# Kernel tuning notes

Measured on AMD Instinct MI355X. Metric: run time of the kernel, lower is better.

The kernel has to match this reference:

```python
import jax, jax.numpy as jnp
import numpy as np
import math

L, D, H = 4, 256, 8
HD = D // H
B, SQ, SK = 2, 1024, 1024
FF = 3 * D
EPS = 1e-5


def setup_inputs() -> dict:
    key = jax.random.key(0)
    ks = jax.random.split(key, 16)
    s = 0.02
    w = lambda k, shape: jax.random.normal(k, shape, jnp.float32) * s
    return {
        "pose": jax.random.normal(ks[0], (B, SQ, D), jnp.float32),
        "vel": jax.random.normal(ks[1], (B, SK, D), jnp.float32),
        "img": jax.random.normal(ks[2], (B, SK, D), jnp.float32),
        "Wq": w(ks[3], (L, D, D)), "bq": jnp.zeros((L, D), jnp.float32),
        "Wk": w(ks[4], (L, D, D)), "bk": jnp.zeros((L, D), jnp.float32),
        "Wv": w(ks[5], (L, D, D)), "bv": jnp.zeros((L, D), jnp.float32),
        "Wo": w(ks[6], (L, D, D)), "bo": jnp.zeros((L, D), jnp.float32),
        "an_g": jnp.ones((L, D), jnp.float32), "an_b": jnp.zeros((L, D), jnp.float32),
        "W1": w(ks[7], (L, D, FF)), "b1": jnp.zeros((L, FF), jnp.float32),
        "W2": w(ks[8], (L, FF, D)), "b2": jnp.zeros((L, D), jnp.float32),
        "fn_g": jnp.ones((L, D), jnp.float32), "fn_b": jnp.zeros((L, D), jnp.float32),
        "n_g": jnp.ones((L, D), jnp.float32), "n_b": jnp.zeros((L, D), jnp.float32),
    }


def entmax15(x):
    # exact alpha=1.5 entmax along the last axis (Peters & Martins 2019)
    x = x * 0.5
    x = x - jnp.max(x, axis=-1, keepdims=True)
    z = -jnp.sort(-x, axis=-1)  # descending
    k = jnp.arange(1, z.shape[-1] + 1, dtype=x.dtype)
    mean = jnp.cumsum(z, axis=-1) / k
    mean_sq = jnp.cumsum(z * z, axis=-1) / k
    ss = k * (mean_sq - mean * mean)
    delta = jnp.clip((1.0 - ss) / k, 0.0)
    tau = mean - jnp.sqrt(delta)
    support = jnp.sum(tau <= z, axis=-1, keepdims=True)  # support size >= 1
    tau_star = jnp.take_along_axis(tau, support - 1, axis=-1)
    p = jnp.clip(x - tau_star, 0.0)
    return p * p


def layer_norm(x, g, b):
    m = jnp.mean(x, axis=-1, keepdims=True)
    v = jnp.mean((x - m) ** 2, axis=-1, keepdims=True)
    return (x - m) * jax.lax.rsqrt(v + EPS) * g + b


def mish(x):
    return x * jnp.tanh(jax.nn.softplus(x))


def reference(pose, vel, img, Wq, bq, Wk, bk, Wv, bv, Wo, bo, an_g, an_b,
              W1, b1, W2, b2, fn_g, fn_b, n_g, n_b):
    def mha(q_in, kv, i):
        bs, sq, _ = q_in.shape
        sk = kv.shape[1]
        q = (q_in @ Wq[i] + bq[i]).reshape(bs, sq, H, HD)
        k = (kv @ Wk[i] + bk[i]).reshape(bs, sk, H, HD)
        v = (kv @ Wv[i] + bv[i]).reshape(bs, sk, H, HD)
        scores = jnp.einsum('bqhd,bkhd->bhqk', q, k) / math.sqrt(HD)
        attn = entmax15(scores)
        out = jnp.einsum('bhqk,bkhd->bqhd', attn, v).reshape(bs, sq, D)
        return out @ Wo[i] + bo[i]

    def cross_layer(x1, x2, i):
        y = layer_norm(mha(x1, x2, i), an_g[i], an_b[i])
        x1 = x1 + y
        y = layer_norm(x1, fn_g[i], fn_b[i])
        h = mish(y @ W1[i] + b1[i]) @ W2[i] + b2[i]
        return x1 + h

    def stack(x, kv):
        for i in range(L):  # small fixed layer loop (shared weights across both paths)
            mem = x
            x = cross_layer(x, kv, i)
            x = layer_norm(x, n_g[i], n_b[i])
            x = x + mem
        return x

    img_out = stack(pose, img)
    pose_out = stack(pose, vel)
    return (pose_out, img_out)
```

## Files before the change

kernel.cpp:

```cpp
#include <hip/hip_runtime.h>
#include <math.h>

#define NL   4
#define DIM  256
#define NH   8
#define HDIM 32
#define SQL  1024
#define SKL  1024
#define FFD  768
#define CB   4
#define ROWS (CB * SQL)

typedef __attribute__((ext_vector_type(8))) short bf16x8;
typedef __attribute__((ext_vector_type(4))) short bf16x4;
typedef __attribute__((ext_vector_type(4))) float f32x4;
typedef __attribute__((ext_vector_type(2))) float f32x2;


__device__ __forceinline__ short f2bf(float f) {
    union { float f; unsigned u; } v; v.f = f;
    unsigned u = v.u + 0x7fffu + ((v.u >> 16) & 1u);
    return (short)(u >> 16);
}

__device__ __forceinline__ float fast_mish(float x) {
    float u = __expf(fminf(x, 20.0f));
    float a = __builtin_fmaf(u, u, 2.0f * u);
    return x * a * __builtin_amdgcn_rcpf(a + 2.0f);
}

__device__ __forceinline__ f32x2 lo2(f32x4 v) { return __builtin_shufflevector(v, v, 0, 1); }
__device__ __forceinline__ f32x2 hi2(f32x4 v) { return __builtin_shufflevector(v, v, 2, 3); }


__global__ __launch_bounds__(256) void init_kernel(
        const float* __restrict__ pose, const float* __restrict__ vel,
        const float* __restrict__ img, float* __restrict__ X,
        short* __restrict__ Xb, short* __restrict__ KVb) {
    int idx = blockIdx.x * 256 + threadIdx.x;
    if (idx >= CB * SQL * DIM) return;
    int c = idx / (SQL * DIM);
    int rem = idx - c * (SQL * DIM);
    int b = c & 1;
    float pv = pose[b * SQL * DIM + rem];
    X[idx]  = pv;
    Xb[idx] = f2bf(pv);
    const float* kv = (c < 2) ? vel : img;
    KVb[idx] = f2bf(kv[b * SQL * DIM + rem]);
}


__global__ __launch_bounds__(256) void transpose_all(
        const float* __restrict__ Wq, const float* __restrict__ Wk,
        const float* __restrict__ Wv, const float* __restrict__ Wo,
        const float* __restrict__ W1, const float* __restrict__ W2,
        short* __restrict__ Wqt, short* __restrict__ Wkt,
        short* __restrict__ Wvt, short* __restrict__ Wot,
        short* __restrict__ W1t, short* __restrict__ W2t) {
    __shared__ float tile[64][65];
    int z = blockIdx.x;
    const float* src; short* dst; int K, N, tx, ty;
    if (z < 256) {
        int m = z >> 6, lyr = (z >> 4) & 3, r = z & 15;
        src = ((m == 0) ? Wq : (m == 1) ? Wk : (m == 2) ? Wv : Wo) + (size_t)lyr * DIM * DIM;
        dst = ((m == 0) ? Wqt : (m == 1) ? Wkt : (m == 2) ? Wvt : Wot) + (size_t)lyr * DIM * DIM;
        K = DIM; N = DIM; tx = r & 3; ty = r >> 2;
    } else if (z < 448) {
        int idx = z - 256, lyr = idx / 48, r = idx % 48;
        src = W1 + (size_t)lyr * DIM * FFD; dst = W1t + (size_t)lyr * DIM * FFD;
        K = DIM; N = FFD; tx = r % 12; ty = r / 12;
    } else {
        int idx = z - 448, lyr = idx / 48, r = idx % 48;
        src = W2 + (size_t)lyr * FFD * DIM; dst = W2t + (size_t)lyr * FFD * DIM;
        K = FFD; N = DIM; tx = r % 4; ty = r / 4;
    }
    int t = threadIdx.x;
    int n0 = tx * 64, k0 = ty * 64;
#pragma unroll
    for (int i = 0; i < 16; i++) {
        int idx = t + i * 256;
        int r = idx >> 6, c = idx & 63;
        tile[r][c] = src[(size_t)(k0 + r) * N + n0 + c];
    }
    __syncthreads();
#pragma unroll
    for (int i = 0; i < 16; i++) {
        int idx = t + i * 256;
        int r = idx >> 6, c = idx & 63;
        dst[(size_t)(n0 + r) * K + k0 + c] = f2bf(tile[c][r]);
    }
}


__global__ __launch_bounds__(256) void qkv_gemm(
        const short* __restrict__ Xb, const short* __restrict__ KVb,
        const short* __restrict__ Wqt, const short* __restrict__ Wkt,
        const short* __restrict__ Wvt,
        const float* __restrict__ bq, const float* __restrict__ bk,
        const float* __restrict__ bv,
        short* __restrict__ Qb, short* __restrict__ Kb, short* __restrict__ Vt,
        float qscale) {
    int z = blockIdx.z;
    const short* A    = (z == 0) ? Xb : KVb;
    const short* Wt   = (z == 0) ? Wqt : (z == 1) ? Wkt : Wvt;
    const float* bias = (z == 0) ? bq : (z == 1) ? bk : bv;
    float scale = (z == 0) ? qscale : 1.0f;

    int t = threadIdx.x, l = t & 63, w = t >> 6;
    int lq = l & 15, lg = l >> 4;
    int bm = blockIdx.y * 64, bn = blockIdx.x * 64;

    const short* ap = A + (size_t)(bm + w * 16 + lq) * DIM + lg * 8;
    const short* wp = Wt + (size_t)(bn + lq) * DIM + lg * 8;

    f32x4 acc[4];
#pragma unroll
    for (int nt = 0; nt < 4; nt++) acc[nt] = (f32x4){0.f, 0.f, 0.f, 0.f};
#pragma unroll
    for (int k0 = 0; k0 < DIM; k0 += 32) {
        bf16x8 af = *(const bf16x8*)(ap + k0);
#pragma unroll
        for (int nt = 0; nt < 4; nt++) {
            bf16x8 bfr = *(const bf16x8*)(wp + (size_t)nt * 16 * DIM + k0);
            acc[nt] = __builtin_amdgcn_mfma_f32_16x16x32_bf16(af, bfr, acc[nt], 0, 0, 0);
        }
    }

    int ms = bm + w * 16 + lg * 4;
#pragma unroll
    for (int nt = 0; nt < 4; nt++) {
        int col = bn + nt * 16 + lq;
        float bv_ = bias[col];
        float v[4];
#pragma unroll
        for (int j = 0; j < 4; j++) v[j] = acc[nt][j] + bv_;
        if (z < 2) {
            short* out = (z == 0) ? Qb : Kb;
#pragma unroll
            for (int j = 0; j < 4; j++) out[(size_t)(ms + j) * DIM + col] = f2bf(v[j] * scale);
        } else {
            int cc = ms >> 10, kl = ms & 1023;
            bf16x4 pk;
#pragma unroll
            for (int j = 0; j < 4; j++) pk[j] = f2bf(v[j]);
            *(bf16x4*)(Vt + ((size_t)(cc * DIM + col)) * SKL + kl) = pk;
        }
    }
}


__global__ __launch_bounds__(512) void gemm_ln2(
        const short* __restrict__ A, const short* __restrict__ Wt,
        const float* __restrict__ bias, const float* __restrict__ Xres,
        const float* __restrict__ ag, const float* __restrict__ ab,
        const float* __restrict__ fg, const float* __restrict__ fb,
        float* __restrict__ x1out, short* __restrict__ yout) {
    __shared__ float gbuf[16][264];
    int t = threadIdx.x, l = t & 63, w = t >> 6;
    int lq = l & 15, lg = l >> 4;
    int bm = blockIdx.x * 16;

    const short* ap = A + (size_t)(bm + lq) * DIM + lg * 8;
    const short* wp = Wt + (size_t)(w * 32 + lq) * DIM + lg * 8;

    f32x4 acc[2];
    acc[0] = (f32x4){0.f, 0.f, 0.f, 0.f};
    acc[1] = (f32x4){0.f, 0.f, 0.f, 0.f};
#pragma unroll
    for (int k0 = 0; k0 < DIM; k0 += 32) {
        bf16x8 af = *(const bf16x8*)(ap + k0);
#pragma unroll
        for (int nt = 0; nt < 2; nt++) {
            bf16x8 bfr = *(const bf16x8*)(wp + (size_t)nt * 16 * DIM + k0);
            acc[nt] = __builtin_amdgcn_mfma_f32_16x16x32_bf16(af, bfr, acc[nt], 0, 0, 0);
        }
    }
#pragma unroll
    for (int nt = 0; nt < 2; nt++) {
        int col = w * 32 + nt * 16 + lq;
        float bv_ = bias[col];
#pragma unroll
        for (int j = 0; j < 4; j++) gbuf[lg * 4 + j][col] = acc[nt][j] + bv_;
    }
    __syncthreads();

    int g = t >> 5, u = t & 31;
    int row = bm + g;
    float s = 0.f, s2 = 0.f;
#pragma unroll
    for (int i = 0; i < 8; i++) {
        float v = gbuf[g][u + 32 * i];
        s += v; s2 += v * v;
    }
#pragma unroll
    for (int off = 1; off < 32; off <<= 1) { s += __shfl_xor(s, off); s2 += __shfl_xor(s2, off); }
    float m = s * (1.f / DIM);
    float rstd = rsqrtf(s2 * (1.f / DIM) - m * m + 1e-5f);

    float x1v[8];
    float sb = 0.f, sb2 = 0.f;
#pragma unroll
    for (int i = 0; i < 8; i++) {
        int col = u + 32 * i;
        float x1 = Xres[(size_t)row * DIM + col] + (gbuf[g][col] - m) * rstd * ag[col] + ab[col];
        x1v[i] = x1; sb += x1; sb2 += x1 * x1;
    }
#pragma unroll
    for (int off = 1; off < 32; off <<= 1) { sb += __shfl_xor(sb, off); sb2 += __shfl_xor(sb2, off); }
    float m2 = sb * (1.f / DIM);
    float rstd2 = rsqrtf(sb2 * (1.f / DIM) - m2 * m2 + 1e-5f);
#pragma unroll
    for (int i = 0; i < 8; i++) {
        int col = u + 32 * i;
        x1out[(size_t)row * DIM + col] = x1v[i];
        yout[(size_t)row * DIM + col]  = f2bf((x1v[i] - m2) * rstd2 * fg[col] + fb[col]);
    }
}


__global__ __launch_bounds__(512) void gemm_ffn(
        const short* __restrict__ Yb, const short* __restrict__ W1t,
        const float* __restrict__ b1, const short* __restrict__ W2t,
        const float* __restrict__ b2, const float* __restrict__ x1res,
        const float* __restrict__ Xres, const float* __restrict__ g_,
        const float* __restrict__ b_,
        float* __restrict__ outf, short* __restrict__ outb) {
    __shared__ __align__(16) char lds[16 * 776 * 2];
    short (*g1)[776]   = (short(*)[776])lds;
    float (*gbuf)[264] = (float(*)[264])lds;

    int t = threadIdx.x, l = t & 63, w = t >> 6;
    int lq = l & 15, lg = l >> 4;
    int bm = blockIdx.x * 16;

    {
        const short* ap = Yb + (size_t)(bm + lq) * DIM + lg * 8;
        const short* wp = W1t + (size_t)(w * 96 + lq) * DIM + lg * 8;
        f32x4 acc[6];
#pragma unroll
        for (int nt = 0; nt < 6; nt++) acc[nt] = (f32x4){0.f, 0.f, 0.f, 0.f};
#pragma unroll
        for (int k0 = 0; k0 < DIM; k0 += 32) {
            bf16x8 af = *(const bf16x8*)(ap + k0);
#pragma unroll
            for (int nt = 0; nt < 6; nt++) {
                bf16x8 bfr = *(const bf16x8*)(wp + (size_t)nt * 16 * DIM + k0);
                acc[nt] = __builtin_amdgcn_mfma_f32_16x16x32_bf16(af, bfr, acc[nt], 0, 0, 0);
            }
        }
#pragma unroll
        for (int nt = 0; nt < 6; nt++) {
            int col = w * 96 + nt * 16 + lq;
            float bv_ = b1[col];
#pragma unroll
            for (int j = 0; j < 4; j++)
                g1[lg * 4 + j][col] = f2bf(fast_mish(acc[nt][j] + bv_));
        }
    }
    __syncthreads();

    f32x4 acc2[2];
    acc2[0] = (f32x4){0.f, 0.f, 0.f, 0.f};
    acc2[1] = (f32x4){0.f, 0.f, 0.f, 0.f};
    {
        const short* wp2 = W2t + (size_t)(w * 32 + lq) * FFD + lg * 8;
#pragma unroll 6
        for (int ks = 0; ks < 24; ks++) {
            bf16x8 af = *(const bf16x8*)(&g1[lq][ks * 32 + lg * 8]);
#pragma unroll
            for (int nt = 0; nt < 2; nt++) {
                bf16x8 bfr = *(const bf16x8*)(wp2 + (size_t)nt * 16 * FFD + ks * 32);
                acc2[nt] = __builtin_amdgcn_mfma_f32_16x16x32_bf16(af, bfr, acc2[nt], 0, 0, 0);
            }
        }
    }
    __syncthreads();

#pragma unroll
    for (int nt = 0; nt < 2; nt++) {
        int col = w * 32 + nt * 16 + lq;
        float bv_ = b2[col];
#pragma unroll
        for (int j = 0; j < 4; j++) {
            int row = bm + lg * 4 + j;
            gbuf[lg * 4 + j][col] = acc2[nt][j] + bv_ + x1res[(size_t)row * DIM + col];
        }
    }
    __syncthreads();

    int g = t >> 5, u = t & 31;
    int row = bm + g;
    float s = 0.f, s2 = 0.f;
#pragma unroll
    for (int i = 0; i < 8; i++) {
        float v = gbuf[g][u + 32 * i];
        s += v; s2 += v * v;
    }
#pragma unroll
    for (int off = 1; off < 32; off <<= 1) { s += __shfl_xor(s, off); s2 += __shfl_xor(s2, off); }
    float m = s * (1.f / DIM);
    float rstd = rsqrtf(s2 * (1.f / DIM) - m * m + 1e-5f);
#pragma unroll
    for (int i = 0; i < 8; i++) {
        int col = u + 32 * i;
        float o = Xres[(size_t)row * DIM + col] + (gbuf[g][col] - m) * rstd * g_[col] + b_[col];
        outf[(size_t)row * DIM + col] = o;
        if (outb) outb[(size_t)row * DIM + col] = f2bf(o);
    }
}


__global__ __launch_bounds__(256) void attn_mfma(
        const short* __restrict__ Q, const short* __restrict__ K,
        const short* __restrict__ Vt, short* __restrict__ O) {
    int h = blockIdx.y, c = blockIdx.z;
    int qbase = blockIdx.x * 16;
    int t = threadIdx.x, l = t & 63, w = t >> 6;
    int lq = l & 15, lg = l >> 4;

    __shared__ __align__(16) short p_lds[4][1024];
    __shared__ float obuf[4][512];
    __shared__ float redf[2][3][4][16];

    bf16x8 qfrag = *(const bf16x8*)(Q + ((size_t)(c * SQL + qbase + lq)) * DIM + h * HDIM + lg * 8);

    const int kw = w * 256;
    f32x4 acc[16];
#pragma unroll
    for (int kt = 0; kt < 16; kt++) {
        bf16x8 kf = *(const bf16x8*)(K + ((size_t)(c * SKL + kw + kt * 16 + lq)) * DIM + h * HDIM + lg * 8);
        f32x4 z = {0.f, 0.f, 0.f, 0.f};
        acc[kt] = __builtin_amdgcn_mfma_f32_16x16x32_bf16(kf, qfrag, z, 0, 0, 0);
    }

    const f32x2 z2  = {0.f, 0.f};
    const f32x2 big = {1e30f, 1e30f};
    const f32x2 one = {1.f, 1.f};

    f32x2 mm = lo2(acc[0]);
#pragma unroll
    for (int kt = 0; kt < 16; kt++) {
        mm = __builtin_elementwise_max(mm, lo2(acc[kt]));
        mm = __builtin_elementwise_max(mm, hi2(acc[kt]));
    }
    float m = fmaxf(mm.x, mm.y);
    m = fmaxf(m, __shfl_xor(m, 16));
    m = fmaxf(m, __shfl_xor(m, 32));
    if (l < 16) redf[1][0][w][l] = m;
    __syncthreads();
    m = fmaxf(fmaxf(redf[1][0][0][lq], redf[1][0][1][lq]),
              fmaxf(redf[1][0][2][lq], redf[1][0][3][lq]));

    float tau = m - 1.0f;
    int r = 0;
    for (;;) {
        f32x2 vt = {tau, tau};
        f32x2 S1 = z2, S2 = z2, NN = z2;
#pragma unroll
        for (int kt = 0; kt < 16; kt++) {
            f32x2 y0 = __builtin_elementwise_max(lo2(acc[kt]) - vt, z2);
            f32x2 y1 = __builtin_elementwise_max(hi2(acc[kt]) - vt, z2);
            S1 += y0; S1 += y1;
            S2 += y0 * y0; S2 += y1 * y1;
            NN += __builtin_elementwise_min(y0 * big, one);
            NN += __builtin_elementwise_min(y1 * big, one);
        }
        float sy = S1.x + S1.y, sy2 = S2.x + S2.y, nn = NN.x + NN.y;
        sy  += __shfl_xor(sy, 16);  sy  += __shfl_xor(sy, 32);
        sy2 += __shfl_xor(sy2, 16); sy2 += __shfl_xor(sy2, 32);
        nn  += __shfl_xor(nn, 16);  nn  += __shfl_xor(nn, 32);
        int b = r & 1;
        if (l < 16) { redf[b][0][w][l] = nn; redf[b][1][w][l] = sy; redf[b][2][w][l] = sy2; }
        __syncthreads();
        nn  = redf[b][0][0][lq] + redf[b][0][1][lq] + redf[b][0][2][lq] + redf[b][0][3][lq];
        sy  = redf[b][1][0][lq] + redf[b][1][1][lq] + redf[b][1][2][lq] + redf[b][1][3][lq];
        sy2 = redf[b][2][0][lq] + redf[b][2][1][lq] + redf[b][2][2][lq] + redf[b][2][3][lq];
        float disc = fmaxf(sy * sy - nn * (sy2 - 1.0f), 0.f);
        float delta = (sy - sqrtf(disc)) / nn;
        tau = fminf(tau + delta, m - 0.03125f);
        r++;
        if (r >= 6 || __all(delta < 1e-6f)) break;
    }

    f32x4 o0 = {0.f, 0.f, 0.f, 0.f}, o1 = {0.f, 0.f, 0.f, 0.f};
    const short* vbase0 = Vt + ((size_t)(c * DIM + h * HDIM + lq)) * SKL;
    const short* vbase1 = vbase0 + (size_t)16 * SKL;
    {
        f32x2 vt = {tau, tau};
        int swz = (lq & 7) << 4;
#pragma unroll
        for (int c2 = 0; c2 < 4; c2++) {
#pragma unroll
            for (int k4 = 0; k4 < 4; k4++) {
                int kt = c2 * 4 + k4;
                f32x2 y0 = __builtin_elementwise_max(lo2(acc[kt]) - vt, z2);
                f32x2 y1 = __builtin_elementwise_max(hi2(acc[kt]) - vt, z2);
                f32x2 p0 = y0 * y0, p1 = y1 * y1;
                unsigned u01, u23;
                asm("v_cvt_pk_bf16_f32 %0, %1, %2" : "=v"(u01) : "v"(p0.x), "v"(p0.y));
                asm("v_cvt_pk_bf16_f32 %0, %1, %2" : "=v"(u23) : "v"(p1.x), "v"(p1.y));
                int klocal = k4 * 16 + lg * 4;
                int byte = lq * 128 + ((klocal * 2) ^ swz);
                *(uint2*)((char*)p_lds[w] + byte) = make_uint2(u01, u23);
            }
#pragma unroll
            for (int k2 = 0; k2 < 2; k2++) {
                int klocal0 = k2 * 32 + lg * 8;
                int byte = lq * 128 + ((klocal0 * 2) ^ swz);
                bf16x8 pa = *(const bf16x8*)((const char*)p_lds[w] + byte);
                int k0 = kw + c2 * 64 + klocal0;
                bf16x8 vb0 = *(const bf16x8*)(vbase0 + k0);
                bf16x8 vb1 = *(const bf16x8*)(vbase1 + k0);
                o0 = __builtin_amdgcn_mfma_f32_16x16x32_bf16(pa, vb0, o0, 0, 0, 0);
                o1 = __builtin_amdgcn_mfma_f32_16x16x32_bf16(pa, vb1, o1, 0, 0, 0);
            }
        }
    }

#pragma unroll
    for (int j = 0; j < 4; j++) {
        obuf[w][(lg * 4 + j) * 32 + lq]      = o0[j];
        obuf[w][(lg * 4 + j) * 32 + 16 + lq] = o1[j];
    }
    __syncthreads();
#pragma unroll
    for (int rep = 0; rep < 2; rep++) {
        int e = t + rep * 256;
        int q = e >> 5, d = e & 31;
        float s = obuf[0][e] + obuf[1][e] + obuf[2][e] + obuf[3][e];
        O[((size_t)(c * SQL + qbase + q)) * DIM + h * HDIM + d] = f2bf(s);
    }
}


extern "C" void kernel_launch(void* const* d_in, const int* in_sizes, int n_in,
                              void* d_out, int out_size, void* d_ws, size_t ws_size,
                              hipStream_t stream) {
    const float* pose = (const float*)d_in[0];
    const float* vel  = (const float*)d_in[1];
    const float* img  = (const float*)d_in[2];
    const float* Wq   = (const float*)d_in[3];
    const float* bq   = (const float*)d_in[4];
    const float* Wk   = (const float*)d_in[5];
    const float* bk   = (const float*)d_in[6];
    const float* Wv   = (const float*)d_in[7];
    const float* bv   = (const float*)d_in[8];
    const float* Wo   = (const float*)d_in[9];
    const float* bo   = (const float*)d_in[10];
    const float* an_g = (const float*)d_in[11];
    const float* an_b = (const float*)d_in[12];
    const float* W1   = (const float*)d_in[13];
    const float* b1   = (const float*)d_in[14];
    const float* W2   = (const float*)d_in[15];
    const float* b2   = (const float*)d_in[16];
    const float* fn_g = (const float*)d_in[17];
    const float* fn_b = (const float*)d_in[18];
    const float* n_g  = (const float*)d_in[19];
    const float* n_b  = (const float*)d_in[20];

    const size_t SZ = (size_t)ROWS * DIM;
    float* X    = (float*)d_ws;
    float* X1b  = X + SZ;
    short* Xb   = (short*)(X1b + SZ);
    short* KVb  = Xb + SZ;
    short* T1b  = KVb + SZ;
    short* Qb   = T1b + SZ;
    short* Kb   = Qb + SZ;
    short* Vt   = Kb + SZ;
    short* Yb   = Vt + SZ;
    short* Wqt  = Yb + SZ;
    short* Wkt  = Wqt + (size_t)NL * DIM * DIM;
    short* Wvt  = Wkt + (size_t)NL * DIM * DIM;
    short* Wot  = Wvt + (size_t)NL * DIM * DIM;
    short* W1t  = Wot + (size_t)NL * DIM * DIM;
    short* W2t  = W1t + (size_t)NL * DIM * FFD;

    {
        int total = CB * SQL * DIM;
        init_kernel<<<(total + 255) / 256, 256, 0, stream>>>(pose, vel, img, X, Xb, KVb);
    }
    transpose_all<<<640, 256, 0, stream>>>(Wq, Wk, Wv, Wo, W1, W2,
                                           Wqt, Wkt, Wvt, Wot, W1t, W2t);

    const float qscale = 0.08838834764831845f;

    for (int i = 0; i < NL; i++) {
        const short* Wqt_i = Wqt + (size_t)i * DIM * DIM;
        const short* Wkt_i = Wkt + (size_t)i * DIM * DIM;
        const short* Wvt_i = Wvt + (size_t)i * DIM * DIM;
        const short* Wot_i = Wot + (size_t)i * DIM * DIM;
        const short* W1t_i = W1t + (size_t)i * DIM * FFD;
        const short* W2t_i = W2t + (size_t)i * DIM * FFD;

        qkv_gemm<<<dim3(DIM / 64, ROWS / 64, 3), 256, 0, stream>>>(
            Xb, KVb, Wqt_i, Wkt_i, Wvt_i,
            bq + i * DIM, bk + i * DIM, bv + i * DIM, Qb, Kb, Vt, qscale);

        attn_mfma<<<dim3(SQL / 16, NH, CB), 256, 0, stream>>>(Qb, Kb, Vt, T1b);

        gemm_ln2<<<ROWS / 16, 512, 0, stream>>>(
            T1b, Wot_i, bo + i * DIM, X,
            an_g + i * DIM, an_b + i * DIM, fn_g + i * DIM, fn_b + i * DIM,
            X1b, Yb);

        float* outp  = (i == NL - 1) ? (float*)d_out : X;
        short* outbp = (i == NL - 1) ? nullptr : Xb;
        gemm_ffn<<<ROWS / 16, 512, 0, stream>>>(
            Yb, W1t_i, b1 + i * FFD, W2t_i, b2 + i * DIM, X1b, X,
            n_g + i * DIM, n_b + i * DIM, outp, outbp);
    }

    (void)in_sizes; (void)n_in; (void)out_size; (void)ws_size;
}
```

Measured before the change: 415.2 us.

## Fuse out-projection LayerNorm and FFN into one tail kernel

Merges the Wo GEMM plus double LayerNorm kernel with the FFN kernel, keeping x1 and the normalized activations in LDS instead of round-tripping them through global memory. This removes one launch per layer and the X1b/Yb workspace traffic. The fused kernel uses more LDS per block, which may reduce occupancy. The attention kernel also gets a launch_bounds occupancy hint of 4.

New measurement: 388.5 us. 1.07x faster.

```diff
diff --git a/kernel.cpp b/kernel.cpp
--- a/kernel.cpp
+++ b/kernel.cpp
@@ -149,99 +149,92 @@
 }
 
 
-__global__ __launch_bounds__(512) void gemm_ln2(
-        const short* __restrict__ A, const short* __restrict__ Wt,
-        const float* __restrict__ bias, const float* __restrict__ Xres,
+__global__ __launch_bounds__(512) void fused_tail(
+        const short* __restrict__ T1b, const short* __restrict__ Wot,
+        const float* __restrict__ bo, const float* __restrict__ Xres,
         const float* __restrict__ ag, const float* __restrict__ ab,
         const float* __restrict__ fg, const float* __restrict__ fb,
-        float* __restrict__ x1out, short* __restrict__ yout) {
+        const short* __restrict__ W1t, const float* __restrict__ b1,
+        const short* __restrict__ W2t, const float* __restrict__ b2,
+        const float* __restrict__ g_, const float* __restrict__ b_,
+        float* __restrict__ outf, short* __restrict__ outb) {
     __shared__ float gbuf[16][264];
+    __shared__ __align__(16) short y_lds[16][280];
+    __shared__ __align__(16) short g1[16][792];
+    float (*xbuf)[264] = (float(*)[264])g1;
+
     int t = threadIdx.x, l = t & 63, w = t >> 6;
     int lq = l & 15, lg = l >> 4;
     int bm = blockIdx.x * 16;
 
-    const short* ap = A + (size_t)(bm + lq) * DIM + lg * 8;
-    const short* wp = Wt + (size_t)(w * 32 + lq) * DIM + lg * 8;
-
-    f32x4 acc[2];
-    acc[0] = (f32x4){0.f, 0.f, 0.f, 0.f};
-    acc[1] = (f32x4){0.f, 0.f, 0.f, 0.f};
-#pragma unroll
-    for (int k0 = 0; k0 < DIM; k0 += 32) {
-        bf16x8 af = *(const bf16x8*)(ap + k0);
+    {
+        const short* ap = T1b + (size_t)(bm + lq) * DIM + lg * 8;
+        const short* wp = Wot + (size_t)(w * 32 + lq) * DIM + lg * 8;
+        f32x4 acc[2];
+        acc[0] = (f32x4){0.f, 0.f, 0.f, 0.f};
+        acc[1] = (f32x4){0.f, 0.f, 0.f, 0.f};
+#pragma unroll
+        for (int k0 = 0; k0 < DIM; k0 += 32) {
+            bf16x8 af = *(const bf16x8*)(ap + k0);
+#pragma unroll
+            for (int nt = 0; nt < 2; nt++) {
+                bf16x8 bfr = *(const bf16x8*)(wp + (size_t)nt * 16 * DIM + k0);
+                acc[nt] = __builtin_amdgcn_mfma_f32_16x16x32_bf16(af, bfr, acc[nt], 0, 0, 0);
+            }
+        }
 #pragma unroll
         for (int nt = 0; nt < 2; nt++) {
-            bf16x8 bfr = *(const bf16x8*)(wp + (size_t)nt * 16 * DIM + k0);
-            acc[nt] = __builtin_amdgcn_mfma_f32_16x16x32_bf16(af, bfr, acc[nt], 0, 0, 0);
-        }
-    }
-#pragma unroll
-    for (int nt = 0; nt < 2; nt++) {
-        int col = w * 32 + nt * 16 + lq;
-        float bv_ = bias[col];
-#pragma unroll
-        for (int j = 0; j < 4; j++) gbuf[lg * 4 + j][col] = acc[nt][j] + bv_;
-    }
-    __syncthreads();
-
-    int g = t >> 5, u = t & 31;
-    int row = bm + g;
-    float s = 0.f, s2 = 0.f;
-#pragma unroll
-    for (int i = 0; i < 8; i++) {
-        float v = gbuf[g][u + 32 * i];
-        s += v; s2 += v * v;
-    }
-#pragma unroll
-    for (int off = 1; off < 32; off <<= 1) { s += __shfl_xor(s, off); s2 += __shfl_xor(s2, off); }
-    float m = s * (1.f / DIM);
-    float rstd = rsqrtf(s2 * (1.f / DIM) - m * m + 1e-5f);
-
-    float x1v[8];
-    float sb = 0.f, sb2 = 0.f;
-#pragma unroll
-    for (int i = 0; i < 8; i++) {
-        int col = u + 32 * i;
-        float x1 = Xres[(size_t)row * DIM + col] + (gbuf[g][col] - m) * rstd * ag[col] + ab[col];
-        x1v[i] = x1; sb += x1; sb2 += x1 * x1;
-    }
-#pragma unroll
-    for (int off = 1; off < 32; off <<= 1) { sb += __shfl_xor(sb, off); sb2 += __shfl_xor(sb2, off); }
-    float m2 = sb * (1.f / DIM);
-    float rstd2 = rsqrtf(sb2 * (1.f / DIM) - m2 * m2 + 1e-5f);
-#pragma unroll
-    for (int i = 0; i < 8; i++) {
-        int col = u + 32 * i;
-        x1out[(size_t)row * DIM + col] = x1v[i];
-        yout[(size_t)row * DIM + col]  = f2bf((x1v[i] - m2) * rstd2 * fg[col] + fb[col]);
-    }
-}
-
-
-__global__ __launch_bounds__(512) void gemm_ffn(
-        const short* __restrict__ Yb, const short* __restrict__ W1t,
-        const float* __restrict__ b1, const short* __restrict__ W2t,
-        const float* __restrict__ b2, const float* __restrict__ x1res,
-        const float* __restrict__ Xres, const float* __restrict__ g_,
-        const float* __restrict__ b_,
-        float* __restrict__ outf, short* __restrict__ outb) {
-    __shared__ __align__(16) char lds[16 * 776 * 2];
-    short (*g1)[776]   = (short(*)[776])lds;
-    float (*gbuf)[264] = (float(*)[264])lds;
-
-    int t = threadIdx.x, l = t & 63, w = t >> 6;
-    int lq = l & 15, lg = l >> 4;
-    int bm = blockIdx.x * 16;
-
-    {
-        const short* ap = Yb + (size_t)(bm + lq) * DIM + lg * 8;
+            int col = w * 32 + nt * 16 + lq;
+            float bv_ = bo[col];
+#pragma unroll
+            for (int j = 0; j < 4; j++) gbuf[lg * 4 + j][col] = acc[nt][j] + bv_;
+        }
+    }
+    __syncthreads();
+
+    {
+        int g = t >> 5, u = t & 31;
+        int row = bm + g;
+        float s = 0.f, s2 = 0.f;
+#pragma unroll
+        for (int i = 0; i < 8; i++) {
+            float v = gbuf[g][u + 32 * i];
+            s += v; s2 += v * v;
+        }
+#pragma unroll
+        for (int off = 1; off < 32; off <<= 1) { s += __shfl_xor(s, off); s2 += __shfl_xor(s2, off); }
+        float m = s * (1.f / DIM);
+        float rstd = rsqrtf(s2 * (1.f / DIM) - m * m + 1e-5f);
+
+        float x1v[8];
+        float sb = 0.f, sb2 = 0.f;
+#pragma unroll
+        for (int i = 0; i < 8; i++) {
+            int col = u + 32 * i;
+            float x1 = Xres[(size_t)row * DIM + col] + (gbuf[g][col] - m) * rstd * ag[col] + ab[col];
+            x1v[i] = x1; sb += x1; sb2 += x1 * x1;
+        }
+#pragma unroll
+        for (int off = 1; off < 32; off <<= 1) { sb += __shfl_xor(sb, off); sb2 += __shfl_xor(sb2, off); }
+        float m2 = sb * (1.f / DIM);
+        float rstd2 = rsqrtf(sb2 * (1.f / DIM) - m2 * m2 + 1e-5f);
+#pragma unroll
+        for (int i = 0; i < 8; i++) {
+            int col = u + 32 * i;
+            gbuf[g][col]  = x1v[i];
+            y_lds[g][col] = f2bf((x1v[i] - m2) * rstd2 * fg[col] + fb[col]);
+        }
+    }
+    __syncthreads();
+
+    {
         const short* wp = W1t + (size_t)(w * 96 + lq) * DIM + lg * 8;
         f32x4 acc[6];
 #pragma unroll
         for (int nt = 0; nt < 6; nt++) acc[nt] = (f32x4){0.f, 0.f, 0.f, 0.f};
 #pragma unroll
         for (int k0 = 0; k0 < DIM; k0 += 32) {
-            bf16x8 af = *(const bf16x8*)(ap + k0);
+            bf16x8 af = *(const bf16x8*)(&y_lds[lq][k0 + lg * 8]);
 #pragma unroll
             for (int nt = 0; nt < 6; nt++) {
                 bf16x8 bfr = *(const bf16x8*)(wp + (size_t)nt * 16 * DIM + k0);
@@ -275,42 +268,41 @@
         }
     }
     __syncthreads();
-
 #pragma unroll
     for (int nt = 0; nt < 2; nt++) {
         int col = w * 32 + nt * 16 + lq;
         float bv_ = b2[col];
 #pragma unroll
-        for (int j = 0; j < 4; j++) {
-            int row = bm + lg * 4 + j;
-            gbuf[lg * 4 + j][col] = acc2[nt][j] + bv_ + x1res[(size_t)row * DIM + col];
-        }
-    }
-    __syncthreads();
-
-    int g = t >> 5, u = t & 31;
-    int row = bm + g;
-    float s = 0.f, s2 = 0.f;
-#pragma unroll
-    for (int i = 0; i < 8; i++) {
-        float v = gbuf[g][u + 32 * i];
-        s += v; s2 += v * v;
-    }
-#pragma unroll
-    for (int off = 1; off < 32; off <<= 1) { s += __shfl_xor(s, off); s2 += __shfl_xor(s2, off); }
-    float m = s * (1.f / DIM);
-    float rstd = rsqrtf(s2 * (1.f / DIM) - m * m + 1e-5f);
-#pragma unroll
-    for (int i = 0; i < 8; i++) {
-        int col = u + 32 * i;
-        float o = Xres[(size_t)row * DIM + col] + (gbuf[g][col] - m) * rstd * g_[col] + b_[col];
-        outf[(size_t)row * DIM + col] = o;
-        if (outb) outb[(size_t)row * DIM + col] = f2bf(o);
-    }
-}
-
-
-__global__ __launch_bounds__(256) void attn_mfma(
+        for (int j = 0; j < 4; j++)
+            xbuf[lg * 4 + j][col] = acc2[nt][j] + bv_ + gbuf[lg * 4 + j][col];
+    }
+    __syncthreads();
+
+    {
+        int g = t >> 5, u = t & 31;
+        int row = bm + g;
+        float s = 0.f, s2 = 0.f;
+#pragma unroll
+        for (int i = 0; i < 8; i++) {
+            float v = xbuf[g][u + 32 * i];
+            s += v; s2 += v * v;
+        }
+#pragma unroll
+        for (int off = 1; off < 32; off <<= 1) { s += __shfl_xor(s, off); s2 += __shfl_xor(s2, off); }
+        float m = s * (1.f / DIM);
+        float rstd = rsqrtf(s2 * (1.f / DIM) - m * m + 1e-5f);
+#pragma unroll
+        for (int i = 0; i < 8; i++) {
+            int col = u + 32 * i;
+            float o = Xres[(size_t)row * DIM + col] + (xbuf[g][col] - m) * rstd * g_[col] + b_[col];
+            outf[(size_t)row * DIM + col] = o;
+            if (outb) outb[(size_t)row * DIM + col] = f2bf(o);
+        }
+    }
+}
+
+
+__global__ __launch_bounds__(256, 4) void attn_mfma(
         const short* __restrict__ Q, const short* __restrict__ K,
         const short* __restrict__ Vt, short* __restrict__ O) {
     int h = blockIdx.y, c = blockIdx.z;
@@ -460,15 +452,13 @@
 
     const size_t SZ = (size_t)ROWS * DIM;
     float* X    = (float*)d_ws;
-    float* X1b  = X + SZ;
-    short* Xb   = (short*)(X1b + SZ);
+    short* Xb   = (short*)(X + SZ);
     short* KVb  = Xb + SZ;
     short* T1b  = KVb + SZ;
     short* Qb   = T1b + SZ;
     short* Kb   = Qb + SZ;
     short* Vt   = Kb + SZ;
-    short* Yb   = Vt + SZ;
-    short* Wqt  = Yb + SZ;
+    short* Wqt  = Vt + SZ;
     short* Wkt  = Wqt + (size_t)NL * DIM * DIM;
     short* Wvt  = Wkt + (size_t)NL * DIM * DIM;
     short* Wot  = Wvt + (size_t)NL * DIM * DIM;
@@ -498,15 +488,12 @@
 
         attn_mfma<<<dim3(SQL / 16, NH, CB), 256, 0, stream>>>(Qb, Kb, Vt, T1b);
 
-        gemm_ln2<<<ROWS / 16, 512, 0, stream>>>(
+        float* outp  = (i == NL - 1) ? (float*)d_out : X;
+        short* outbp = (i == NL - 1) ? nullptr : Xb;
+        fused_tail<<<ROWS / 16, 512, 0, stream>>>(
             T1b, Wot_i, bo + i * DIM, X,
             an_g + i * DIM, an_b + i * DIM, fn_g + i * DIM, fn_b + i * DIM,
-            X1b, Yb);
-
-        float* outp  = (i == NL - 1) ? (float*)d_out : X;
-        short* outbp = (i == NL - 1) ? nullptr : Xb;
-        gemm_ffn<<<ROWS / 16, 512, 0, stream>>>(
-            Yb, W1t_i, b1 + i * FFD, W2t_i, b2 + i * DIM, X1b, X,
+            W1t_i, b1 + i * FFD, W2t_i, b2 + i * DIM,
             n_g + i * DIM, n_b + i * DIM, outp, outbp);
     }
 
```
